# Performance work log

Measured on AMD Instinct MI355X. Metric: run time of the kernel, lower is better.

Reference implementation:

```python
import jax, jax.numpy as jnp
import numpy as np

B, S, T = 32, 64, 64          # batch, src_len, tgt_len
E, H, V = 512, 1024, 32000    # embed, hidden, vocab
WSCALE = 0.05                 # keep tanh/sigmoid in sane range


def setup_inputs() -> dict:
    key = jax.random.key(0)
    ks = jax.random.split(key, 14)
    n = lambda k, shp: jax.random.normal(k, shp, jnp.float32)
    return {
        "target": jax.random.randint(ks[0], (B, T), 0, V),
        "src_enc": n(ks[1], (B, S, 2 * H)),
        "h0": n(ks[2], (B, H)),
        "c0": n(ks[3], (B, H)),
        "emb": n(ks[4], (V, E)) * WSCALE,
        "W_ih": n(ks[5], (E, 4 * H)) * WSCALE,
        "W_hh": n(ks[6], (H, 4 * H)) * WSCALE,
        "b_rnn": jnp.zeros((4 * H,), jnp.float32),
        "W_attn": n(ks[7], (2 * H, H)) * WSCALE,
        "b_attn": jnp.zeros((H,), jnp.float32),
        "W_comb": n(ks[8], (2 * H, H)) * WSCALE,
        "b_comb": jnp.zeros((H,), jnp.float32),
        "W_out": n(ks[9], (H, V)) * WSCALE,
        "b_out": jnp.zeros((V,), jnp.float32),
    }


def reference(target, src_enc, h0, c0, emb, W_ih, W_hh, b_rnn,
              W_attn, b_attn, W_comb, b_comb, W_out, b_out):
    # Pre-project encoder states once (decode() applies attention.linear up front)
    enc_proj = src_enc @ W_attn + b_attn                 # [B,S,H]
    xs = emb[target[:, :-1]]                             # teacher forcing [B,T-1,E]
    xs = jnp.swapaxes(xs, 0, 1)                          # [T-1,B,E] for scan

    def step(carry, x_t):
        h, c = carry
        # LSTM cell (torch gate order i, f, g, o)
        gates = x_t @ W_ih + h @ W_hh + b_rnn            # [B,4H]
        i, f, g, o = jnp.split(gates, 4, axis=-1)
        c = jax.nn.sigmoid(f) * c + jax.nn.sigmoid(i) * jnp.tanh(g)
        h = jax.nn.sigmoid(o) * jnp.tanh(c)
        # Bilinear attention: score = h^T (W_attn e_s) over source positions
        scores = jnp.einsum('bsh,bh->bs', enc_proj, h)
        attn = jax.nn.softmax(scores, axis=-1)
        ctx = jnp.einsum('bs,bsh->bh', attn, enc_proj)   # [B,H]
        out = jnp.tanh(jnp.concatenate([h, ctx], axis=-1) @ W_comb + b_comb)
        return (h, c), out

    _, outs = jax.lax.scan(step, (h0, c0), xs)           # [T-1,B,H]
    outs = jnp.swapaxes(outs, 0, 1)                      # [B,T-1,H]
    logits = outs @ W_out + b_out                        # [B,T-1,V]
    return logits
```

## Files before the change

kernel.cpp:

```cpp
#include <hip/hip_runtime.h>
#include <stdint.h>

#define NB    32
#define NS    64
#define TDEC  63
#define NE    512
#define NH    1024
#define NV    32000

typedef float  floatx4 __attribute__((ext_vector_type(4)));
typedef short  short8  __attribute__((ext_vector_type(8)));
typedef short  short4v __attribute__((ext_vector_type(4)));

__device__ __forceinline__ float bf2f(short s) {
  return __uint_as_float(((uint32_t)(uint16_t)s) << 16);
}
__device__ __forceinline__ short f2bf(float f) {
  uint32_t u = __float_as_uint(f);
  uint32_t r = (u + 0x7fffu + ((u >> 16) & 1u)) >> 16;
  return (short)(uint16_t)r;
}
__device__ __forceinline__ float sigm(float x) { return 1.f / (1.f + expf(-x)); }

__device__ __forceinline__ int xcd_swz(int orig, int nwg) {
  return (orig & 7) * (nwg >> 3) + (orig >> 3);
}

__device__ __forceinline__ void tr_plain(
    const float* __restrict__ W, short* __restrict__ Wt, int K, int N,
    int bx, int by, int perm, float (*tile)[33], int tid)
{
  int k0 = bx * 32, n0 = by * 32;
  int tx = tid & 31, ty = tid >> 5;
#pragma unroll
  for (int r = 0; r < 32; r += 8)
    tile[ty + r][tx] = W[(size_t)(k0 + ty + r) * N + n0 + tx];
  __syncthreads();
  int kq = tid & 7, nl = tid >> 3;
  int n = n0 + nl;
  int rr = perm ? ((n & 1023) * 4 + (n >> 10)) : n;
  short4v v;
#pragma unroll
  for (int q = 0; q < 4; ++q) v[q] = f2bf(tile[kq * 4 + q][nl]);
  *(short4v*)&Wt[(size_t)rr * K + k0 + kq * 4] = v;
}

__device__ __forceinline__ void tr_split(
    const float* __restrict__ W, short* __restrict__ Wt_hi, short* __restrict__ Wt_lo,
    int K, int N, int bx, int by, int perm, float (*tile)[33], int tid)
{
  int k0 = bx * 32, n0 = by * 32;
  int tx = tid & 31, ty = tid >> 5;
#pragma unroll
  for (int r = 0; r < 32; r += 8)
    tile[ty + r][tx] = W[(size_t)(k0 + ty + r) * N + n0 + tx];
  __syncthreads();
  int kq = tid & 7, nl = tid >> 3;
  int n = n0 + nl;
  int rr = perm ? ((n & 1023) * 4 + (n >> 10)) : n;
  short4v vh, vl;
#pragma unroll
  for (int q = 0; q < 4; ++q) {
    float v = tile[kq * 4 + q][nl];
    short h = f2bf(v);
    vh[q] = h;
    vl[q] = f2bf(v - bf2f(h));
  }
  size_t o = (size_t)rr * K + k0 + kq * 4;
  *(short4v*)&Wt_hi[o] = vh;
  *(short4v*)&Wt_lo[o] = vl;
}

__global__ __launch_bounds__(256) void prep_all(
    const float* __restrict__ Wattn, const float* __restrict__ Wih,
    const float* __restrict__ Whh,   const float* __restrict__ Wcomb,
    const float* __restrict__ Wout,
    const int* __restrict__ target,  const float* __restrict__ emb,
    const float* __restrict__ h0,    const float* __restrict__ c0,
    const float* __restrict__ brnn,  const float* __restrict__ src,
    short* __restrict__ WattnTh, short* __restrict__ WattnTl,
    short* __restrict__ WihTp,
    short* __restrict__ WhpHi,   short* __restrict__ WhpLo,
    short* __restrict__ WcTHi,   short* __restrict__ WcTLo,
    short* __restrict__ WoutT,
    short* __restrict__ xs, float* __restrict__ hf_all,
    short* __restrict__ hhi_all, short* __restrict__ hlo_all,
    float* __restrict__ c_buf, float* __restrict__ brnn_p,
    short* __restrict__ sAh, short* __restrict__ sAl)
{
  __shared__ float tile[32][33];
  const int blk = blockIdx.x;
  const int tid = threadIdx.x;

  if (blk < 2048) {
    tr_split(Wattn, WattnTh, WattnTl, 2048, 1024, blk & 63, blk >> 6, 0, tile, tid);
  } else if (blk < 4096) {
    int b = blk - 2048;
    tr_plain(Wih, WihTp, 512, 4096, b & 15, b >> 4, 1, tile, tid);
  } else if (blk < 8192) {
    int b = blk - 4096;
    tr_split(Whh, WhpHi, WhpLo, 1024, 4096, b & 31, b >> 5, 1, tile, tid);
  } else if (blk < 10240) {
    int b = blk - 8192;
    tr_split(Wcomb, WcTHi, WcTLo, 2048, 1024, b & 63, b >> 6, 0, tile, tid);
  } else if (blk < 42240) {
    int b = blk - 10240;
    tr_plain(Wout, WoutT, 1024, 32000, b & 31, b >> 5, 0, tile, tid);
  } else {
    const int NXS = TDEC * NB * NE;
    const int HN = NH * NB;
    const int NSRC = 2048 * 2048;
    int total = NXS + 2 * HN + 4096 + NSRC;
    int b = blk - 42240;
    for (int idx = b * 256 + tid; idx < total; idx += 2048 * 256) {
      if (idx < NXS) {
        int row = idx >> 9, e = idx & 511;
        int t = row >> 5, bb = row & 31;
        int token = target[bb * 64 + t];
        xs[idx] = f2bf(emb[(size_t)token * NE + e]);
      } else if (idx < NXS + HN) {
        int r = idx - NXS;
        float v = h0[r];
        hf_all[r] = v;
        short hh = f2bf(v);
        hhi_all[r] = hh;
        hlo_all[r] = f2bf(v - bf2f(hh));
      } else if (idx < NXS + 2 * HN) {
        int r = idx - NXS - HN;
        c_buf[r] = c0[r];
      } else if (idx < NXS + 2 * HN + 4096) {
        int c = idx - NXS - 2 * HN;
        brnn_p[c] = brnn[(c & 3) * 1024 + (c >> 2)];
      } else {
        int e = idx - NXS - 2 * HN - 4096;
        float v = src[e];
        short h = f2bf(v);
        sAh[e] = h;
        sAl[e] = f2bf(v - bf2f(h));
      }
    }
  }
}

template<int OUT_BF, int SWZ>
__global__ __launch_bounds__(256) void gemm_kernel(
    const short* __restrict__ Ab, const short* __restrict__ Bt,
    void* __restrict__ Cptr, const float* __restrict__ bias,
    int M, int N, int K)
{
  __shared__ char smem[2 * 128 * 72 * 2];
  short* As = (short*)smem;
  short* Bs = (short*)(smem + 128 * 72 * 2);
  float* cst = (float*)smem;
  int tile_id = blockIdx.y * gridDim.x + blockIdx.x;
  if (SWZ) tile_id = xcd_swz(tile_id, gridDim.x * gridDim.y);
  const int m0 = (tile_id % gridDim.x) * 128;
  const int n0 = (tile_id / gridDim.x) * 128;
  const int tid = threadIdx.x;
  const int lane = tid & 63;
  const int wid = tid >> 6;
  const int wr = wid >> 1, wc = wid & 1;

  floatx4 acc[4][4] = {};
  const int row = tid >> 1;
  const int ks  = (tid & 1) << 5;

  for (int k0 = 0; k0 < K; k0 += 64) {
    {
      int gm = m0 + row;
      short8 v0, v1, v2, v3;
      if (gm < M) {
        const short* src = Ab + (size_t)gm * K + k0 + ks;
        v0 = *(const short8*)src;
        v1 = *(const short8*)(src + 8);
        v2 = *(const short8*)(src + 16);
        v3 = *(const short8*)(src + 24);
      } else {
#pragma unroll
        for (int c = 0; c < 8; ++c) { v0[c] = 0; v1[c] = 0; v2[c] = 0; v3[c] = 0; }
      }
      *(short8*)&As[row * 72 + ks]      = v0;
      *(short8*)&As[row * 72 + ks + 8]  = v1;
      *(short8*)&As[row * 72 + ks + 16] = v2;
      *(short8*)&As[row * 72 + ks + 24] = v3;
    }
    {
      const short* src = Bt + (size_t)(n0 + row) * K + k0 + ks;
      *(short8*)&Bs[row * 72 + ks]      = *(const short8*)src;
      *(short8*)&Bs[row * 72 + ks + 8]  = *(const short8*)(src + 8);
      *(short8*)&Bs[row * 72 + ks + 16] = *(const short8*)(src + 16);
      *(short8*)&Bs[row * 72 + ks + 24] = *(const short8*)(src + 24);
    }
    __syncthreads();

    const int kA = (lane >> 4) << 3;
    const int rsel = lane & 15;
#pragma unroll
    for (int kk = 0; kk < 64; kk += 32) {
      short8 af[4], bfr[4];
#pragma unroll
      for (int mi = 0; mi < 4; ++mi)
        af[mi] = *(const short8*)&As[(wr * 64 + mi * 16 + rsel) * 72 + kk + kA];
#pragma unroll
      for (int ni = 0; ni < 4; ++ni)
        bfr[ni] = *(const short8*)&Bs[(wc * 64 + ni * 16 + rsel) * 72 + kk + kA];
#pragma unroll
      for (int mi = 0; mi < 4; ++mi)
#pragma unroll
        for (int ni = 0; ni < 4; ++ni)
          acc[mi][ni] = __builtin_amdgcn_mfma_f32_16x16x32_bf16(af[mi], bfr[ni], acc[mi][ni], 0, 0, 0);
    }
    __syncthreads();
  }

  const int crow = (lane >> 4) * 4;
  const int ccol = lane & 15;
  if (OUT_BF) {
#pragma unroll
    for (int mi = 0; mi < 4; ++mi) {
#pragma unroll
      for (int ni = 0; ni < 4; ++ni) {
        int gn = n0 + wc * 64 + ni * 16 + ccol;
        float bv = bias[gn];
#pragma unroll
        for (int i = 0; i < 4; ++i) {
          int gm = m0 + wr * 64 + mi * 16 + crow + i;
          if (gm < M)
            __builtin_nontemporal_store(f2bf(acc[mi][ni][i] + bv),
                                        &((short*)Cptr)[(size_t)gm * N + gn]);
        }
      }
    }
  } else {
#pragma unroll
    for (int p = 0; p < 4; ++p) {
      __syncthreads();
      if (wr == (p >> 1)) {
        int mi0 = (p & 1) * 2;
#pragma unroll
        for (int mm = 0; mm < 2; ++mm) {
#pragma unroll
          for (int ni = 0; ni < 4; ++ni) {
            int c = wc * 64 + ni * 16 + ccol;
#pragma unroll
            for (int i = 0; i < 4; ++i)
              cst[(mm * 16 + crow + i) * 132 + c] = acc[mi0 + mm][ni][i];
          }
        }
      }
      __syncthreads();
#pragma unroll
      for (int rep = 0; rep < 4; ++rep) {
        int cell = tid + rep * 256;
        int r = cell >> 5, q = cell & 31;
        int gm = m0 + p * 32 + r;
        int gn = n0 + q * 4;
        if (gm < M) {
          float4 bv = *(const float4*)&bias[gn];
          floatx4 v;
          v[0] = cst[r * 132 + q * 4 + 0] + bv.x;
          v[1] = cst[r * 132 + q * 4 + 1] + bv.y;
          v[2] = cst[r * 132 + q * 4 + 2] + bv.z;
          v[3] = cst[r * 132 + q * 4 + 3] + bv.w;
          __builtin_nontemporal_store(v, (floatx4*)&((float*)Cptr)[(size_t)gm * N + gn]);
        }
      }
    }
  }
}

__global__ __launch_bounds__(256) void gemm_split2(
    const short* __restrict__ Ah, const short* __restrict__ Al,
    const short* __restrict__ Bt_hi, const short* __restrict__ Bt_lo,
    float* __restrict__ C, const float* __restrict__ bias,
    int M, int N, int K)
{
  __shared__ short As_hi[128 * 72];
  __shared__ short As_lo[128 * 72];
  __shared__ short Bs_hi[128 * 72];
  __shared__ short Bs_lo[128 * 72];
  int tile_id = xcd_swz(blockIdx.y * gridDim.x + blockIdx.x, gridDim.x * gridDim.y);
  const int m0 = (tile_id % gridDim.x) * 128;
  const int n0 = (tile_id / gridDim.x) * 128;
  const int tid = threadIdx.x;
  const int lane = tid & 63;
  const int wid = tid >> 6;
  const int wr = wid >> 1, wc = wid & 1;

  floatx4 acc[4][4] = {};
  const int row = tid >> 1;
  const int ks  = (tid & 1) << 5;

  for (int k0 = 0; k0 < K; k0 += 64) {
    {
      size_t o = (size_t)(m0 + row) * K + k0 + ks;
#pragma unroll
      for (int c = 0; c < 4; ++c) {
        *(short8*)&As_hi[row * 72 + ks + c * 8] = *(const short8*)(Ah + o + c * 8);
        *(short8*)&As_lo[row * 72 + ks + c * 8] = *(const short8*)(Al + o + c * 8);
      }
    }
    {
      size_t o = (size_t)(n0 + row) * K + k0 + ks;
#pragma unroll
      for (int c = 0; c < 4; ++c) {
        *(short8*)&Bs_hi[row * 72 + ks + c * 8] = *(const short8*)(Bt_hi + o + c * 8);
        *(short8*)&Bs_lo[row * 72 + ks + c * 8] = *(const short8*)(Bt_lo + o + c * 8);
      }
    }
    __syncthreads();

    const int kA = (lane >> 4) << 3;
    const int rsel = lane & 15;
#pragma unroll
    for (int kk = 0; kk < 64; kk += 32) {
      short8 ah[4], al[4], bh[4], bl[4];
#pragma unroll
      for (int mi = 0; mi < 4; ++mi) {
        int off = (wr * 64 + mi * 16 + rsel) * 72 + kk + kA;
        ah[mi] = *(const short8*)&As_hi[off];
        al[mi] = *(const short8*)&As_lo[off];
      }
#pragma unroll
      for (int ni = 0; ni < 4; ++ni) {
        int off = (wc * 64 + ni * 16 + rsel) * 72 + kk + kA;
        bh[ni] = *(const short8*)&Bs_hi[off];
        bl[ni] = *(const short8*)&Bs_lo[off];
      }
#pragma unroll
      for (int mi = 0; mi < 4; ++mi)
#pragma unroll
        for (int ni = 0; ni < 4; ++ni) {
          floatx4 a = acc[mi][ni];
          a = __builtin_amdgcn_mfma_f32_16x16x32_bf16(al[mi], bh[ni], a, 0, 0, 0);
          a = __builtin_amdgcn_mfma_f32_16x16x32_bf16(ah[mi], bl[ni], a, 0, 0, 0);
          a = __builtin_amdgcn_mfma_f32_16x16x32_bf16(ah[mi], bh[ni], a, 0, 0, 0);
          acc[mi][ni] = a;
        }
    }
    __syncthreads();
  }

  const int crow = (lane >> 4) * 4;
  const int ccol = lane & 15;
#pragma unroll
  for (int mi = 0; mi < 4; ++mi) {
#pragma unroll
    for (int ni = 0; ni < 4; ++ni) {
      int gn = n0 + wc * 64 + ni * 16 + ccol;
      float bv = bias[gn];
#pragma unroll
      for (int i = 0; i < 4; ++i) {
        int gm = m0 + wr * 64 + mi * 16 + crow + i;
        C[(size_t)gm * N + gn] = acc[mi][ni][i] + bv;
      }
    }
  }
}

__global__ __launch_bounds__(512) void scan_a(
    int t,
    const short* __restrict__ Whp_hi,
    const short* __restrict__ Whp_lo,
    const short* __restrict__ gatesx,
    short* __restrict__ hhi_all,
    short* __restrict__ hlo_all,
    float* __restrict__ hf_all,
    float* __restrict__ c_buf)
{
  __shared__ float smem[8 * 32 * 33];
  const int blk = blockIdx.x;
  const int tid = threadIdx.x;
  const int lane = tid & 63;
  const int wid = tid >> 6;
  const int rsel = lane & 15;
  const int kA = (lane >> 4) * 8;
  const int crow = (lane >> 4) * 4;
  const int ccol = lane & 15;

  const size_t spv = (size_t)t * (NH * NB);
  const size_t snw = (size_t)(t + 1) * (NH * NB);
  const short* Hh = hhi_all + spv;
  const short* Hl = hlo_all + spv;
  const int c0 = blk * 32;
  const int kb = wid * 128;

  floatx4 acc[2][2] = {};
  const short* wh0 = Whp_hi + (size_t)(c0 + rsel) * NH + kb + kA;
  const short* wl0 = Whp_lo + (size_t)(c0 + rsel) * NH + kb + kA;
  const short* wh1 = Whp_hi + (size_t)(c0 + 16 + rsel) * NH + kb + kA;
  const short* wl1 = Whp_lo + (size_t)(c0 + 16 + rsel) * NH + kb + kA;
  const short* ha0 = Hh + (size_t)rsel * NH + kb + kA;
  const short* la0 = Hl + (size_t)rsel * NH + kb + kA;
  const short* ha1 = Hh + (size_t)(16 + rsel) * NH + kb + kA;
  const short* la1 = Hl + (size_t)(16 + rsel) * NH + kb + kA;
#pragma unroll
  for (int kk = 0; kk < 4; ++kk) {
    int k0 = kk * 32;
    short8 a0h = *(const short8*)(ha0 + k0);
    short8 a0l = *(const short8*)(la0 + k0);
    short8 a1h = *(const short8*)(ha1 + k0);
    short8 a1l = *(const short8*)(la1 + k0);
    short8 b0h = *(const short8*)(wh0 + k0);
    short8 b0l = *(const short8*)(wl0 + k0);
    short8 b1h = *(const short8*)(wh1 + k0);
    short8 b1l = *(const short8*)(wl1 + k0);
    acc[0][0] = __builtin_amdgcn_mfma_f32_16x16x32_bf16(a0l, b0h, acc[0][0], 0, 0, 0);
    acc[0][0] = __builtin_amdgcn_mfma_f32_16x16x32_bf16(a0h, b0l, acc[0][0], 0, 0, 0);
    acc[0][0] = __builtin_amdgcn_mfma_f32_16x16x32_bf16(a0h, b0h, acc[0][0], 0, 0, 0);
    acc[0][1] = __builtin_amdgcn_mfma_f32_16x16x32_bf16(a0l, b1h, acc[0][1], 0, 0, 0);
    acc[0][1] = __builtin_amdgcn_mfma_f32_16x16x32_bf16(a0h, b1l, acc[0][1], 0, 0, 0);
    acc[0][1] = __builtin_amdgcn_mfma_f32_16x16x32_bf16(a0h, b1h, acc[0][1], 0, 0, 0);
    acc[1][0] = __builtin_amdgcn_mfma_f32_16x16x32_bf16(a1l, b0h, acc[1][0], 0, 0, 0);
    acc[1][0] = __builtin_amdgcn_mfma_f32_16x16x32_bf16(a1h, b0l, acc[1][0], 0, 0, 0);
    acc[1][0] = __builtin_amdgcn_mfma_f32_16x16x32_bf16(a1h, b0h, acc[1][0], 0, 0, 0);
    acc[1][1] = __builtin_amdgcn_mfma_f32_16x16x32_bf16(a1l, b1h, acc[1][1], 0, 0, 0);
    acc[1][1] = __builtin_amdgcn_mfma_f32_16x16x32_bf16(a1h, b1l, acc[1][1], 0, 0, 0);
    acc[1][1] = __builtin_amdgcn_mfma_f32_16x16x32_bf16(a1h, b1h, acc[1][1], 0, 0, 0);
  }
#pragma unroll
  for (int mi = 0; mi < 2; ++mi)
#pragma unroll
    for (int ni = 0; ni < 2; ++ni)
#pragma unroll
      for (int i = 0; i < 4; ++i)
        smem[wid * 1056 + (mi * 16 + crow + i) * 33 + ni * 16 + ccol] = acc[mi][ni][i];
  __syncthreads();
  if (tid < 256) {
    int b = tid & 31, jl = tid >> 5;
    float g[4];
#pragma unroll
    for (int q = 0; q < 4; ++q) {
      float s = 0;
#pragma unroll
      for (int w = 0; w < 8; ++w) s += smem[w * 1056 + b * 33 + jl * 4 + q];
      g[q] = s;
    }
    int jg = (c0 >> 2) + jl;
    const short* gx = gatesx + ((size_t)t * 32 + b) * 4096 + c0 + jl * 4;
    short4v gxv = *(const short4v*)gx;
    float gi = g[0] + bf2f(gxv[0]);
    float gf = g[1] + bf2f(gxv[1]);
    float gg = g[2] + bf2f(gxv[2]);
    float go = g[3] + bf2f(gxv[3]);
    float co = c_buf[b * NH + jg];
    float cn = sigm(gf) * co + sigm(gi) * tanhf(gg);
    float hn = sigm(go) * tanhf(cn);
    c_buf[b * NH + jg] = cn;
    hf_all[snw + b * NH + jg] = hn;
    short hh = f2bf(hn);
    hhi_all[snw + b * NH + jg] = hh;
    hlo_all[snw + b * NH + jg] = f2bf(hn - bf2f(hh));
  }
}

__global__ __launch_bounds__(256) void attn_batch(
    const float* __restrict__ encp,
    const float* __restrict__ hf_all,
    short* __restrict__ ctxhi_all,
    short* __restrict__ ctxlo_all)
{
  __shared__ float h_lds[NH];
  __shared__ float part[4 * 64];
  __shared__ float sc_lds[64];
  __shared__ float p_lds[64];
  const int blk = xcd_swz(blockIdx.x, gridDim.x);
  const int b = blk / TDEC;
  const int t = blk % TDEC;
  const int tid = threadIdx.x;
  const float* h = hf_all + ((size_t)(t + 1) * 32 + b) * NH;

  ((float4*)h_lds)[tid] = ((const float4*)h)[tid];
  __syncthreads();
  {
    int s = tid & 63, kc = tid >> 6;
    const float4* ep = (const float4*)(encp + ((size_t)(b * 64 + s)) * NH + kc * 256);
    const float4* hp = (const float4*)(h_lds + kc * 256);
    float ac0 = 0, ac1 = 0, ac2 = 0, ac3 = 0;
#pragma unroll
    for (int i = 0; i < 64; i += 4) {
      float4 e0 = ep[i],     h0v = hp[i];
      float4 e1 = ep[i + 1], h1v = hp[i + 1];
      float4 e2 = ep[i + 2], h2v = hp[i + 2];
      float4 e3 = ep[i + 3], h3v = hp[i + 3];
      ac0 = fmaf(e0.x, h0v.x, ac0); ac0 = fmaf(e0.y, h0v.y, ac0);
      ac0 = fmaf(e0.z, h0v.z, ac0); ac0 = fmaf(e0.w, h0v.w, ac0);
      ac1 = fmaf(e1.x, h1v.x, ac1); ac1 = fmaf(e1.y, h1v.y, ac1);
      ac1 = fmaf(e1.z, h1v.z, ac1); ac1 = fmaf(e1.w, h1v.w, ac1);
      ac2 = fmaf(e2.x, h2v.x, ac2); ac2 = fmaf(e2.y, h2v.y, ac2);
      ac2 = fmaf(e2.z, h2v.z, ac2); ac2 = fmaf(e2.w, h2v.w, ac2);
      ac3 = fmaf(e3.x, h3v.x, ac3); ac3 = fmaf(e3.y, h3v.y, ac3);
      ac3 = fmaf(e3.z, h3v.z, ac3); ac3 = fmaf(e3.w, h3v.w, ac3);
    }
    part[kc * 64 + s] = (ac0 + ac1) + (ac2 + ac3);
  }
  __syncthreads();
  if (tid < 64) {
    float sc = part[tid] + part[64 + tid] + part[128 + tid] + part[192 + tid];
    sc_lds[tid] = sc;
    float m = sc;
#pragma unroll
    for (int off = 32; off; off >>= 1) m = fmaxf(m, __shfl_xor(m, off));
    float e = expf(sc - m);
    float sum = e;
#pragma unroll
    for (int off = 32; off; off >>= 1) sum += __shfl_xor(sum, off);
    p_lds[tid] = e / sum;
  }
  __syncthreads();
  {
    int k4 = tid * 4;
    float a0 = 0, a1 = 0, a2 = 0, a3 = 0;
    const float* ep = encp + (size_t)(b * 64) * NH + k4;
    for (int s = 0; s < 64; ++s) {
      float p = p_lds[s];
      float4 e = *(const float4*)(ep + (size_t)s * NH);
      a0 = fmaf(p, e.x, a0); a1 = fmaf(p, e.y, a1);
      a2 = fmaf(p, e.z, a2); a3 = fmaf(p, e.w, a3);
    }
    size_t crow = ((size_t)t * 32 + b) * NH + k4;
    short4v c4h, c4l;
    float av[4] = {a0, a1, a2, a3};
#pragma unroll
    for (int q = 0; q < 4; ++q) {
      short hh = f2bf(av[q]);
      c4h[q] = hh;
      c4l[q] = f2bf(av[q] - bf2f(hh));
    }
    *(short4v*)(ctxhi_all + crow) = c4h;
    *(short4v*)(ctxlo_all + crow) = c4l;
  }
}

__global__ __launch_bounds__(256) void gemm_comb(
    const short* __restrict__ Ah_hi,
    const short* __restrict__ Ah_lo,
    const short* __restrict__ Cx_hi,
    const short* __restrict__ Cx_lo,
    const short* __restrict__ Bt_hi,
    const short* __restrict__ Bt_lo,
    const float* __restrict__ bcomb,
    short* __restrict__ outs)
{
  __shared__ short As_hi[128 * 72];
  __shared__ short As_lo[128 * 72];
  __shared__ short Bs_hi[128 * 72];
  __shared__ short Bs_lo[128 * 72];
  int tile_id = xcd_swz(blockIdx.y * gridDim.x + blockIdx.x, gridDim.x * gridDim.y);
  const int m0 = (tile_id % gridDim.x) * 128;
  const int n0 = (tile_id / gridDim.x) * 128;
  const int tid = threadIdx.x;
  const int lane = tid & 63;
  const int wid = tid >> 6;
  const int wr = wid >> 1, wc = wid & 1;

  floatx4 acc[4][4] = {};
  const int row = tid >> 1;
  const int ks  = (tid & 1) << 5;

  for (int k0 = 0; k0 < 2048; k0 += 64) {
    {
      int gr = m0 + row;
      const short* sh;
      const short* sl;
      if (k0 < NH) {
        sh = Ah_hi + (size_t)gr * NH + k0 + ks;
        sl = Ah_lo + (size_t)gr * NH + k0 + ks;
      } else {
        sh = Cx_hi + (size_t)gr * NH + (k0 - NH) + ks;
        sl = Cx_lo + (size_t)gr * NH + (k0 - NH) + ks;
      }
#pragma unroll
      for (int c = 0; c < 4; ++c) {
        *(short8*)&As_hi[row * 72 + ks + c * 8] = *(const short8*)(sh + c * 8);
        *(short8*)&As_lo[row * 72 + ks + c * 8] = *(const short8*)(sl + c * 8);
      }
    }
    {
      size_t o = (size_t)(n0 + row) * 2048 + k0 + ks;
#pragma unroll
      for (int c = 0; c < 4; ++c) {
        *(short8*)&Bs_hi[row * 72 + ks + c * 8] = *(const short8*)(Bt_hi + o + c * 8);
        *(short8*)&Bs_lo[row * 72 + ks + c * 8] = *(const short8*)(Bt_lo + o + c * 8);
      }
    }
    __syncthreads();

    const int kA = (lane >> 4) << 3;
    const int rsel = lane & 15;
#pragma unroll
    for (int kk = 0; kk < 64; kk += 32) {
      short8 ah[4], al[4], bh[4], bl[4];
#pragma unroll
      for (int mi = 0; mi < 4; ++mi) {
        int off = (wr * 64 + mi * 16 + rsel) * 72 + kk + kA;
        ah[mi] = *(const short8*)&As_hi[off];
        al[mi] = *(const short8*)&As_lo[off];
      }
#pragma unroll
      for (int ni = 0; ni < 4; ++ni) {
        int off = (wc * 64 + ni * 16 + rsel) * 72 + kk + kA;
        bh[ni] = *(const short8*)&Bs_hi[off];
        bl[ni] = *(const short8*)&Bs_lo[off];
      }
#pragma unroll
      for (int mi = 0; mi < 4; ++mi)
#pragma unroll
        for (int ni = 0; ni < 4; ++ni) {
          floatx4 a = acc[mi][ni];
          a = __builtin_amdgcn_mfma_f32_16x16x32_bf16(al[mi], bh[ni], a, 0, 0, 0);
          a = __builtin_amdgcn_mfma_f32_16x16x32_bf16(ah[mi], bl[ni], a, 0, 0, 0);
          a = __builtin_amdgcn_mfma_f32_16x16x32_bf16(ah[mi], bh[ni], a, 0, 0, 0);
          acc[mi][ni] = a;
        }
    }
    __syncthreads();
  }

  const int crow = (lane >> 4) * 4;
  const int ccol = lane & 15;
#pragma unroll
  for (int mi = 0; mi < 4; ++mi) {
#pragma unroll
    for (int ni = 0; ni < 4; ++ni) {
      int gn = n0 + wc * 64 + ni * 16 + ccol;
      float bv = bcomb[gn];
#pragma unroll
      for (int i = 0; i < 4; ++i) {
        int gm = m0 + wr * 64 + mi * 16 + crow + i;
        if (gm < TDEC * NB) {
          int tt = gm >> 5, bb = gm & 31;
          outs[((size_t)bb * TDEC + tt) * NH + gn] = f2bf(tanhf(acc[mi][ni][i] + bv));
        }
      }
    }
  }
}

extern "C" void kernel_launch(void* const* d_in, const int* in_sizes, int n_in,
                              void* d_out, int out_size, void* d_ws, size_t ws_size,
                              hipStream_t stream)
{
  const int*   target = (const int*)  d_in[0];
  const float* src    = (const float*)d_in[1];
  const float* h0     = (const float*)d_in[2];
  const float* c0     = (const float*)d_in[3];
  const float* emb    = (const float*)d_in[4];
  const float* Wih    = (const float*)d_in[5];
  const float* Whh    = (const float*)d_in[6];
  const float* brnn   = (const float*)d_in[7];
  const float* Wattn  = (const float*)d_in[8];
  const float* battn  = (const float*)d_in[9];
  const float* Wcomb  = (const float*)d_in[10];
  const float* bcomb  = (const float*)d_in[11];
  const float* Wout   = (const float*)d_in[12];
  const float* bout   = (const float*)d_in[13];
  float* out = (float*)d_out;

  char* ws = (char*)d_ws;
  size_t off = 0;
  auto take = [&](size_t bytes) { char* p = ws + off; off += (bytes + 255) & ~(size_t)255; return p; };
  short* WoutT    = (short*)take((size_t)NV * NH * 2);
  short* WattnTh  = (short*)take((size_t)NH * 2048 * 2);
  short* WattnTl  = (short*)take((size_t)NH * 2048 * 2);
  short* WihTp    = (short*)take((size_t)4096 * NE * 2);
  short* WhpHi    = (short*)take((size_t)4096 * NH * 2);
  short* WhpLo    = (short*)take((size_t)4096 * NH * 2);
  short* WcTHi    = (short*)take((size_t)NH * 2048 * 2);
  short* WcTLo    = (short*)take((size_t)NH * 2048 * 2);
  short* xs_bf    = (short*)take((size_t)TDEC * NB * NE * 2);
  float* encp     = (float*)take((size_t)NB * NS * NH * 4);
  short* gatesx   = (short*)take((size_t)TDEC * NB * 4096 * 2);
  short* outs_bf  = (short*)take((size_t)TDEC * NB * NH * 2);
  float* hf_all   = (float*)take((size_t)65 * NB * NH * 4);
  short* hhi_all  = (short*)take((size_t)65 * NB * NH * 2);
  short* hlo_all  = (short*)take((size_t)65 * NB * NH * 2);
  short* ctxhi_a  = (short*)take((size_t)2048 * NH * 2);
  short* ctxlo_a  = (short*)take((size_t)2048 * NH * 2);
  float* c_buf    = (float*)take((size_t)NH * NB * 4);
  float* brnn_p   = (float*)take((size_t)4096 * 4);
  short* sAl      = (short*)take((size_t)2048 * 2048 * 2);
  short* sAh      = gatesx;
  if (off > ws_size) return;

  prep_all<<<44288, 256, 0, stream>>>(
      Wattn, Wih, Whh, Wcomb, Wout, target, emb, h0, c0, brnn, src,
      WattnTh, WattnTl, WihTp, WhpHi, WhpLo, WcTHi, WcTLo, WoutT,
      xs_bf, hf_all, hhi_all, hlo_all, c_buf, brnn_p, sAh, sAl);
  gemm_split2<<<dim3(16, NH / 128), 256, 0, stream>>>(
      sAh, sAl, WattnTh, WattnTl, encp, battn, 2048, NH, 2048);
  gemm_kernel<1, 1><<<dim3(16, 4096 / 128), 256, 0, stream>>>(xs_bf, WihTp, gatesx, brnn_p, TDEC * NB, 4096, NE);
  for (int t = 0; t < TDEC; ++t)
    scan_a<<<128, 512, 0, stream>>>(t, WhpHi, WhpLo, gatesx, hhi_all, hlo_all, hf_all, c_buf);
  attn_batch<<<TDEC * NB, 256, 0, stream>>>(encp, hf_all, ctxhi_a, ctxlo_a);
  gemm_comb<<<dim3(16, 8), 256, 0, stream>>>(hhi_all + (size_t)32 * NH, hlo_all + (size_t)32 * NH,
                                             ctxhi_a, ctxlo_a, WcTHi, WcTLo, bcomb, outs_bf);
  gemm_kernel<0, 1><<<dim3(16, NV / 128), 256, 0, stream>>>(outs_bf, WoutT, out, bout, TDEC * NB, NV, NH);
}
```

Measured before the change: 1.202 ms.

## Overlap W_out and W_comb transposes with latency-bound LSTM scan steps

Moves the W_out bf16 transpose and the W_comb hi/lo split-transpose out of the prep kernel. They are spread across the 63 scan_a launches as extra blocks (indices 128 and up), so that otherwise idle CUs do this work while the 128 recurrence blocks run. The intent is to hide about 34k tile-transpose blocks behind the latency-bound sequential scan. The risk is that the extra blocks compete for bandwidth or CU slots with the critical scan blocks and slow each step.

```diff
diff --git a/kernel.cpp b/kernel.cpp
--- a/kernel.cpp
+++ b/kernel.cpp
@@ -73,16 +73,13 @@
 
 __global__ __launch_bounds__(256) void prep_all(
     const float* __restrict__ Wattn, const float* __restrict__ Wih,
-    const float* __restrict__ Whh,   const float* __restrict__ Wcomb,
-    const float* __restrict__ Wout,
+    const float* __restrict__ Whh,
     const int* __restrict__ target,  const float* __restrict__ emb,
     const float* __restrict__ h0,    const float* __restrict__ c0,
     const float* __restrict__ brnn,  const float* __restrict__ src,
     short* __restrict__ WattnTh, short* __restrict__ WattnTl,
     short* __restrict__ WihTp,
     short* __restrict__ WhpHi,   short* __restrict__ WhpLo,
-    short* __restrict__ WcTHi,   short* __restrict__ WcTLo,
-    short* __restrict__ WoutT,
     short* __restrict__ xs, float* __restrict__ hf_all,
     short* __restrict__ hhi_all, short* __restrict__ hlo_all,
     float* __restrict__ c_buf, float* __restrict__ brnn_p,
@@ -100,18 +97,12 @@
   } else if (blk < 8192) {
     int b = blk - 4096;
     tr_split(Whh, WhpHi, WhpLo, 1024, 4096, b & 31, b >> 5, 1, tile, tid);
-  } else if (blk < 10240) {
-    int b = blk - 8192;
-    tr_split(Wcomb, WcTHi, WcTLo, 2048, 1024, b & 63, b >> 6, 0, tile, tid);
-  } else if (blk < 42240) {
-    int b = blk - 10240;
-    tr_plain(Wout, WoutT, 1024, 32000, b & 31, b >> 5, 0, tile, tid);
   } else {
     const int NXS = TDEC * NB * NE;
     const int HN = NH * NB;
     const int NSRC = 2048 * 2048;
     int total = NXS + 2 * HN + 4096 + NSRC;
-    int b = blk - 42240;
+    int b = blk - 8192;
     for (int idx = b * 256 + tid; idx < total; idx += 2048 * 256) {
       if (idx < NXS) {
         int row = idx >> 9, e = idx & 511;
@@ -366,11 +357,68 @@
     short* __restrict__ hhi_all,
     short* __restrict__ hlo_all,
     float* __restrict__ hf_all,
-    float* __restrict__ c_buf)
+    float* __restrict__ c_buf,
+    const float* __restrict__ Wout,  short* __restrict__ WoutT,
+    const float* __restrict__ Wcomb, short* __restrict__ WcTHi,
+    short* __restrict__ WcTLo)
 {
   __shared__ float smem[8 * 32 * 33];
   const int blk = blockIdx.x;
   const int tid = threadIdx.x;
+
+  if (blk >= 128) {
+    float (*tile)[33] = (float(*)[33])smem;
+    if (blk < 636) {
+      int id = t * 508 + (blk - 128);
+      if (id < 32000) {
+        int k0 = (id & 31) * 32, n0 = (id >> 5) * 32;
+        if (tid < 256) {
+          int tx = tid & 31, ty = tid >> 5;
+#pragma unroll
+          for (int r = 0; r < 32; r += 8)
+            tile[ty + r][tx] = Wout[(size_t)(k0 + ty + r) * 32000 + n0 + tx];
+        }
+        __syncthreads();
+        if (tid < 256) {
+          int kq = tid & 7, nl = tid >> 3;
+          int n = n0 + nl;
+          short4v v;
+#pragma unroll
+          for (int q = 0; q < 4; ++q) v[q] = f2bf(tile[kq * 4 + q][nl]);
+          *(short4v*)&WoutT[(size_t)n * 1024 + k0 + kq * 4] = v;
+        }
+      }
+    } else {
+      int id = t * 33 + (blk - 636);
+      if (id < 2048) {
+        int k0 = (id & 63) * 32, n0 = (id >> 6) * 32;
+        if (tid < 256) {
+          int tx = tid & 31, ty = tid >> 5;
+#pragma unroll
+          for (int r = 0; r < 32; r += 8)
+            tile[ty + r][tx] = Wcomb[(size_t)(k0 + ty + r) * 1024 + n0 + tx];
+        }
+        __syncthreads();
+        if (tid < 256) {
+          int kq = tid & 7, nl = tid >> 3;
+          int n = n0 + nl;
+          short4v vh, vl;
+#pragma unroll
+          for (int q = 0; q < 4; ++q) {
+            float v = tile[kq * 4 + q][nl];
+            short h = f2bf(v);
+            vh[q] = h;
+            vl[q] = f2bf(v - bf2f(h));
+          }
+          size_t o = (size_t)n * 2048 + k0 + kq * 4;
+          *(short4v*)&WcTHi[o] = vh;
+          *(short4v*)&WcTLo[o] = vl;
+        }
+      }
+    }
+    return;
+  }
+
   const int lane = tid & 63;
   const int wid = tid >> 6;
   const int rsel = lane & 15;
@@ -683,15 +731,16 @@
   short* sAh      = gatesx;
   if (off > ws_size) return;
 
-  prep_all<<<44288, 256, 0, stream>>>(
-      Wattn, Wih, Whh, Wcomb, Wout, target, emb, h0, c0, brnn, src,
-      WattnTh, WattnTl, WihTp, WhpHi, WhpLo, WcTHi, WcTLo, WoutT,
+  prep_all<<<10240, 256, 0, stream>>>(
+      Wattn, Wih, Whh, target, emb, h0, c0, brnn, src,
+      WattnTh, WattnTl, WihTp, WhpHi, WhpLo,
       xs_bf, hf_all, hhi_all, hlo_all, c_buf, brnn_p, sAh, sAl);
   gemm_split2<<<dim3(16, NH / 128), 256, 0, stream>>>(
       sAh, sAl, WattnTh, WattnTl, encp, battn, 2048, NH, 2048);
   gemm_kernel<1, 1><<<dim3(16, 4096 / 128), 256, 0, stream>>>(xs_bf, WihTp, gatesx, brnn_p, TDEC * NB, 4096, NE);
   for (int t = 0; t < TDEC; ++t)
-    scan_a<<<128, 512, 0, stream>>>(t, WhpHi, WhpLo, gatesx, hhi_all, hlo_all, hf_all, c_buf);
+    scan_a<<<669, 512, 0, stream>>>(t, WhpHi, WhpLo, gatesx, hhi_all, hlo_all,
+                                    hf_all, c_buf, Wout, WoutT, Wcomb, WcTHi, WcTLo);
   attn_batch<<<TDEC * NB, 256, 0, stream>>>(encp, hf_all, ctxhi_a, ctxlo_a);
   gemm_comb<<<dim3(16, 8), 256, 0, stream>>>(hhi_all + (size_t)32 * NH, hlo_all + (size_t)32 * NH,
                                              ctxhi_a, ctxlo_a, WcTHi, WcTLo, bcomb, outs_bf);
```

New measurement: 1.157 ms. 1.04x faster.
